# Performance work log

Hardware: AMD Instinct MI355X
Metric: run time of the kernel (lower is better)

Reference implementation:

```python
import jax, jax.numpy as jnp
import numpy as np

# EISANI constants (inference path, dense non-EI weights, static connections)
NUM_BITS = 16        # EISANITABcontinuousVarEncodingNumBits
K_SYN = 32           # numberOfSynapsesPerSegment
SEGMENTS = 2         # numberOfSegmentsPerNeuron
THETA = 8            # segment activation threshold (synapse-count based)
H = 4096             # hiddenLayerSize
F = 128              # numberOfFeatures
C = 10               # numberOfClasses
B = 64               # batch


def _make_weight(key, h, s, p):
    """Dense weight [h, s, p] with exactly K_SYN nonzero +/-1 synapses per segment
    (mirrors _initialise_layer_weights dense non-EI branch)."""
    k1, k2 = jax.random.split(key)
    cols = jax.random.randint(k1, (h, s, K_SYN), 0, p)
    signs = jnp.where(jax.random.bernoulli(k2, 0.5, (h, s, K_SYN)), 1.0, -1.0).astype(jnp.float32)
    hh = jnp.arange(h)[:, None, None]
    ss = jnp.arange(s)[None, :, None]
    return jnp.zeros((h, s, p), jnp.float32).at[hh, ss, cols].set(signs)


def setup_inputs() -> dict:
    key = jax.random.key(0)
    kx, k0, k1, k2, ko = jax.random.split(key, 5)
    x = jax.random.uniform(kx, (B, F), dtype=jnp.float32)
    W0 = _make_weight(k0, H, SEGMENTS, F * NUM_BITS)
    W1 = _make_weight(k1, H, SEGMENTS, H)
    W2 = _make_weight(k2, H, SEGMENTS, H)
    outW = jax.random.normal(ko, (3, H, C), dtype=jnp.float32) * 0.02
    return {"x": x, "W0": W0, "W1": W1, "W2": W2, "outW": outW}


def _encode(x):
    # thermometer (graded) encoding of continuous vars into NUM_BITS binary bits
    thresholds = (jnp.arange(NUM_BITS, dtype=jnp.float32) + 1.0) / (NUM_BITS + 1.0)
    bits = (x[:, :, None] >= thresholds).astype(jnp.float32)  # [B, F, NUM_BITS]
    return bits.reshape(x.shape[0], -1)  # [B, F*NUM_BITS]


def reference(x, W0, W1, W2, outW):
    acts = _encode(x)  # [B, P0]
    layer_acts = []
    for W in (W0, W1, W2):
        # segment membrane sums over binary presynaptic activations
        z = jnp.einsum('bp,hsp->bhs', acts, W)  # [B, H, S]
        # neuron fires if ANY segment reaches threshold
        fired = jnp.any(z >= THETA, axis=-1)
        acts = fired.astype(jnp.float32)  # binary activation [B, H]
        layer_acts.append(acts)
    stacked = jnp.stack(layer_acts)  # [L, B, H]
    out = jnp.einsum('lbh,lhc->bc', stacked, outW)  # class scores [B, C]
    return out
```

## Files before the change

kernel.cpp:

```cpp
#include <hip/hip_runtime.h>
#include <hip/hip_bf16.h>

typedef unsigned long long u64;

#define H_SZ 4096
#define NBITS 16
#define NFEAT 128
#define NCLS 10
#define THETA 8


__global__ void encode_kernel(const float* __restrict__ x, u64* __restrict__ actp0) {
    int idx = blockIdx.x * blockDim.x + threadIdx.x;
    if (idx >= 32 * 64) return;
    int wword = idx >> 6;
    int b = idx & 63;
    int c = wword >> 2, j = wword & 3;
    u64 word = 0;
    for (int i = 0; i < 64; i++) {
        int p = c * 256 + 4 * i + j;
        int f = p >> 4, t = p & 15;
        float thr = (t + 1.0f) / (NBITS + 1.0f);
        if (x[b * NFEAT + f] >= thr) word |= (1ULL << i);
    }
    actp0[wword * 64 + b] = word;
}

template <int NCH, int ROWS>
__global__ __launch_bounds__(256, 4) void layer_kernel(const float* __restrict__ W,
                                                       const u64* __restrict__ actp,
                                                       u64* __restrict__ ballots) {
    constexpr int NW = NCH * 4;
    constexpr int G = 8;
    constexpr int TG = ROWS * NCH / G;
    __shared__ u64 lds[NW * 64];
    int tid = threadIdx.x;
    for (int i = tid; i < NW * 64; i += 256) lds[i] = actp[i];
    __syncthreads();

    int lane = tid & 63;
    int wave = blockIdx.x * 4 + (tid >> 6);
    int wid0 = wave * ROWS;
    const float4* base = (const float4*)(W + (size_t)wid0 * (NCH * 256)) + lane;

    float4 A[G], B[G];
    #pragma unroll
    for (int k = 0; k < G; k++) A[k] = base[k * 64];

    int z = 0;
    #pragma unroll
    for (int g = 0; g < TG; g++) {
        float4* cur = (g & 1) ? B : A;
        float4* nxt = (g & 1) ? A : B;
        if (g + 1 < TG) {
            #pragma unroll
            for (int k = 0; k < G; k++) nxt[k] = base[((g + 1) * G + k) * 64];
        }
        #pragma unroll
        for (int k = 0; k < G; k++) {
            int c = (g * G + k) % NCH;
            float4 v = cur[k];
            u64 p0 = __ballot(v.x > 0.0f);
            u64 n0 = __ballot(v.x < 0.0f);
            u64 p1 = __ballot(v.y > 0.0f);
            u64 n1 = __ballot(v.y < 0.0f);
            u64 p2 = __ballot(v.z > 0.0f);
            u64 n2 = __ballot(v.z < 0.0f);
            u64 p3 = __ballot(v.w > 0.0f);
            u64 n3 = __ballot(v.w < 0.0f);
            u64 a0 = lds[(c * 4 + 0) * 64 + lane];
            u64 a1 = lds[(c * 4 + 1) * 64 + lane];
            u64 a2 = lds[(c * 4 + 2) * 64 + lane];
            u64 a3 = lds[(c * 4 + 3) * 64 + lane];
            z += __builtin_popcountll(a0 & p0) - __builtin_popcountll(a0 & n0)
               + __builtin_popcountll(a1 & p1) - __builtin_popcountll(a1 & n1)
               + __builtin_popcountll(a2 & p2) - __builtin_popcountll(a2 & n2)
               + __builtin_popcountll(a3 & p3) - __builtin_popcountll(a3 & n3);
        }
        if (((g + 1) * G) % NCH == 0) {
            u64 fz = __ballot(z >= THETA);
            int r = ((g + 1) * G) / NCH - 1;
            if (lane == 0) ballots[wid0 + r] = fz;
            z = 0;
        }
    }
}

__global__ void transpose_kernel(const u64* __restrict__ ballots,
                                 u64* __restrict__ f,
                                 u64* __restrict__ actp) {
    __shared__ u64 lds[256];
    int c = blockIdx.x;
    int tid = threadIdx.x;
    int h = c * 256 + tid;
    u64 fh = ballots[2 * h] | ballots[2 * h + 1];
    f[h] = fh;
    lds[tid] = fh;
    __syncthreads();
    int j = tid >> 6, b = tid & 63;
    u64 word = 0;
    #pragma unroll 8
    for (int i = 0; i < 64; i++)
        word |= ((lds[4 * i + j] >> b) & 1ULL) << i;
    actp[(c * 4 + j) * 64 + b] = word;
}

__global__ void output_kernel(const float* __restrict__ outW,
                              const u64* __restrict__ f,
                              float* __restrict__ out) {
    int tid = threadIdx.x;
    int lane = tid & 63;
    int wid = blockIdx.x * 4 + (tid >> 6);
    int l = wid / (NCLS * 64);
    int rem = wid % (NCLS * 64);
    int c = rem / 64;
    int chunk = rem % 64;
    const u64* fl = f + l * H_SZ;
    int h0 = chunk * 64;
    float acc = 0.0f;
    #pragma unroll 8
    for (int h = h0; h < h0 + 64; h++) {
        float wv = outW[((size_t)(l * H_SZ + h)) * NCLS + c];
        u64 ball = fl[h];
        if ((ball >> lane) & 1ULL) acc += wv;
    }
    atomicAdd(&out[lane * NCLS + c], acc);
}

extern "C" void kernel_launch(void* const* d_in, const int* in_sizes, int n_in,
                              void* d_out, int out_size, void* d_ws, size_t ws_size,
                              hipStream_t stream) {
    const float* x    = (const float*)d_in[0];
    const float* W0   = (const float*)d_in[1];
    const float* W1   = (const float*)d_in[2];
    const float* W2   = (const float*)d_in[3];
    const float* outW = (const float*)d_in[4];
    float* out = (float*)d_out;

    char* ws = (char*)d_ws;
    u64* actp0   = (u64*)(ws);
    u64* actp1   = (u64*)(ws + 16384);
    u64* actp2   = (u64*)(ws + 49152);
    u64* ballots = (u64*)(ws + 81920);
    u64* f       = (u64*)(ws + 147456);
    u64* scratch = (u64*)(ws + 245760);

    hipMemsetAsync(d_out, 0, (size_t)out_size * sizeof(float), stream);

    encode_kernel<<<8, 256, 0, stream>>>(x, actp0);

    layer_kernel<8, 2><<<1024, 256, 0, stream>>>(W0, actp0, ballots);
    transpose_kernel<<<16, 256, 0, stream>>>(ballots, f + 0 * H_SZ, actp1);

    layer_kernel<16, 2><<<1024, 256, 0, stream>>>(W1, actp1, ballots);
    transpose_kernel<<<16, 256, 0, stream>>>(ballots, f + 1 * H_SZ, actp2);

    layer_kernel<16, 2><<<1024, 256, 0, stream>>>(W2, actp2, ballots);
    transpose_kernel<<<16, 256, 0, stream>>>(ballots, f + 2 * H_SZ, scratch);

    output_kernel<<<480, 256, 0, stream>>>(outW, f, out);
}
```

Before: 395.6 us.

## Stream all layer weights in one kernel, compress W1/W2 to sign bitmasks

Replaces the three per-layer weight-streaming kernels with one kernel that computes layer 0 and, in the same launch, converts W1 and W2 into packed positive/negative sign bitmasks that do not depend on earlier activations. Layers 1 and 2 then run a small kernel that reads only the compact masks plus activations from LDS. The goal is to read all weight bytes in one fully parallel pass without dependency stalls between layers, so the later layers become cheap. This adds mask writes to workspace at fixed 4MB/16MB offsets and assumes the workspace is large enough.

```diff
diff --git a/kernel.cpp b/kernel.cpp
--- a/kernel.cpp
+++ b/kernel.cpp
@@ -26,63 +26,137 @@
     actp0[wword * 64 + b] = word;
 }
 
-template <int NCH, int ROWS>
-__global__ __launch_bounds__(256, 4) void layer_kernel(const float* __restrict__ W,
-                                                       const u64* __restrict__ actp,
-                                                       u64* __restrict__ ballots) {
-    constexpr int NW = NCH * 4;
+__global__ __launch_bounds__(256, 4) void stream_kernel(const float* __restrict__ W0,
+                                                        const float* __restrict__ W1,
+                                                        const float* __restrict__ W2,
+                                                        const u64* __restrict__ actp0,
+                                                        u64* __restrict__ ballots,
+                                                        u64* __restrict__ mask1,
+                                                        u64* __restrict__ mask2) {
     constexpr int G = 8;
-    constexpr int TG = ROWS * NCH / G;
-    __shared__ u64 lds[NW * 64];
-    int tid = threadIdx.x;
-    for (int i = tid; i < NW * 64; i += 256) lds[i] = actp[i];
+    __shared__ u64 lds[2048];
+    int tid = threadIdx.x;
+    int lane = tid & 63;
+    int warp = tid >> 6;
+    int bid = blockIdx.x;
+
+    if (bid < 512) {
+        for (int i = tid; i < 2048; i += 256) lds[i] = actp0[i];
+        __syncthreads();
+
+        int wave = bid * 4 + warp;
+        int wid0 = wave * 4;
+        const float4* base = (const float4*)(W0 + (size_t)wid0 * 2048) + lane;
+
+        float4 A[G], B[G];
+        #pragma unroll
+        for (int k = 0; k < G; k++) A[k] = base[k * 64];
+
+        #pragma unroll
+        for (int g = 0; g < 4; g++) {
+            float4* cur = (g & 1) ? B : A;
+            float4* nxt = (g & 1) ? A : B;
+            if (g + 1 < 4) {
+                #pragma unroll
+                for (int k = 0; k < G; k++) nxt[k] = base[((g + 1) * G + k) * 64];
+            }
+            int z = 0;
+            #pragma unroll
+            for (int k = 0; k < G; k++) {
+                float4 v = cur[k];
+                u64 p0 = __ballot(v.x > 0.0f);
+                u64 n0 = __ballot(v.x < 0.0f);
+                u64 p1 = __ballot(v.y > 0.0f);
+                u64 n1 = __ballot(v.y < 0.0f);
+                u64 p2 = __ballot(v.z > 0.0f);
+                u64 n2 = __ballot(v.z < 0.0f);
+                u64 p3 = __ballot(v.w > 0.0f);
+                u64 n3 = __ballot(v.w < 0.0f);
+                u64 a0 = lds[(k * 4 + 0) * 64 + lane];
+                u64 a1 = lds[(k * 4 + 1) * 64 + lane];
+                u64 a2 = lds[(k * 4 + 2) * 64 + lane];
+                u64 a3 = lds[(k * 4 + 3) * 64 + lane];
+                z += __builtin_popcountll(a0 & p0) - __builtin_popcountll(a0 & n0)
+                   + __builtin_popcountll(a1 & p1) - __builtin_popcountll(a1 & n1)
+                   + __builtin_popcountll(a2 & p2) - __builtin_popcountll(a2 & n2)
+                   + __builtin_popcountll(a3 & p3) - __builtin_popcountll(a3 & n3);
+            }
+            u64 fz = __ballot(z >= THETA);
+            if (lane == 0) ballots[wid0 + g] = fz;
+        }
+    } else {
+        const float* Wsrc = (bid < 1536) ? W1 : W2;
+        u64* masks = (bid < 1536) ? mask1 : mask2;
+        int wave = ((bid < 1536) ? (bid - 512) : (bid - 1536)) * 4 + warp;
+        size_t c0 = (size_t)wave * 32;
+        const float4* base = (const float4*)Wsrc + c0 * 64 + lane;
+
+        float4 A[G], B[G];
+        #pragma unroll
+        for (int k = 0; k < G; k++) A[k] = base[k * 64];
+
+        #pragma unroll
+        for (int g = 0; g < 4; g++) {
+            float4* cur = (g & 1) ? B : A;
+            float4* nxt = (g & 1) ? A : B;
+            if (g + 1 < 4) {
+                #pragma unroll
+                for (int k = 0; k < G; k++) nxt[k] = base[((g + 1) * G + k) * 64];
+            }
+            #pragma unroll
+            for (int k = 0; k < G; k++) {
+                float4 v = cur[k];
+                u64 m0 = __ballot(v.x > 0.0f);
+                u64 m1 = __ballot(v.x < 0.0f);
+                u64 m2 = __ballot(v.y > 0.0f);
+                u64 m3 = __ballot(v.y < 0.0f);
+                u64 m4 = __ballot(v.z > 0.0f);
+                u64 m5 = __ballot(v.z < 0.0f);
+                u64 m6 = __ballot(v.w > 0.0f);
+                u64 m7 = __ballot(v.w < 0.0f);
+                u64 w = m0;
+                w = (lane == 1) ? m1 : w;
+                w = (lane == 2) ? m2 : w;
+                w = (lane == 3) ? m3 : w;
+                w = (lane == 4) ? m4 : w;
+                w = (lane == 5) ? m5 : w;
+                w = (lane == 6) ? m6 : w;
+                w = (lane == 7) ? m7 : w;
+                if (lane < 8) masks[(c0 + g * G + k) * 8 + lane] = w;
+            }
+        }
+    }
+}
+
+__global__ __launch_bounds__(256) void mask_layer_kernel(const u64* __restrict__ masks,
+                                                         const u64* __restrict__ actp,
+                                                         u64* __restrict__ ballots) {
+    __shared__ u64 am[4096];
+    __shared__ u64 mm[2048];
+    int tid = threadIdx.x;
+    int r0 = blockIdx.x * 16;
+    for (int i = tid; i < 4096; i += 256) am[i] = actp[i];
+    for (int i = tid; i < 2048; i += 256) mm[i] = masks[(size_t)r0 * 128 + i];
     __syncthreads();
 
     int lane = tid & 63;
-    int wave = blockIdx.x * 4 + (tid >> 6);
-    int wid0 = wave * ROWS;
-    const float4* base = (const float4*)(W + (size_t)wid0 * (NCH * 256)) + lane;
-
-    float4 A[G], B[G];
+    int warp = tid >> 6;
     #pragma unroll
-    for (int k = 0; k < G; k++) A[k] = base[k * 64];
-
-    int z = 0;
-    #pragma unroll
-    for (int g = 0; g < TG; g++) {
-        float4* cur = (g & 1) ? B : A;
-        float4* nxt = (g & 1) ? A : B;
-        if (g + 1 < TG) {
+    for (int rr = 0; rr < 4; rr++) {
+        int local = warp * 4 + rr;
+        int z = 0;
+        #pragma unroll
+        for (int c = 0; c < 16; c++) {
             #pragma unroll
-            for (int k = 0; k < G; k++) nxt[k] = base[((g + 1) * G + k) * 64];
+            for (int j = 0; j < 4; j++) {
+                u64 p = mm[local * 128 + c * 8 + j * 2];
+                u64 n = mm[local * 128 + c * 8 + j * 2 + 1];
+                u64 a = am[(c * 4 + j) * 64 + lane];
+                z += __builtin_popcountll(a & p) - __builtin_popcountll(a & n);
+            }
         }
-        #pragma unroll
-        for (int k = 0; k < G; k++) {
-            int c = (g * G + k) % NCH;
-            float4 v = cur[k];
-            u64 p0 = __ballot(v.x > 0.0f);
-            u64 n0 = __ballot(v.x < 0.0f);
-            u64 p1 = __ballot(v.y > 0.0f);
-            u64 n1 = __ballot(v.y < 0.0f);
-            u64 p2 = __ballot(v.z > 0.0f);
-            u64 n2 = __ballot(v.z < 0.0f);
-            u64 p3 = __ballot(v.w > 0.0f);
-            u64 n3 = __ballot(v.w < 0.0f);
-            u64 a0 = lds[(c * 4 + 0) * 64 + lane];
-            u64 a1 = lds[(c * 4 + 1) * 64 + lane];
-            u64 a2 = lds[(c * 4 + 2) * 64 + lane];
-            u64 a3 = lds[(c * 4 + 3) * 64 + lane];
-            z += __builtin_popcountll(a0 & p0) - __builtin_popcountll(a0 & n0)
-               + __builtin_popcountll(a1 & p1) - __builtin_popcountll(a1 & n1)
-               + __builtin_popcountll(a2 & p2) - __builtin_popcountll(a2 & n2)
-               + __builtin_popcountll(a3 & p3) - __builtin_popcountll(a3 & n3);
-        }
-        if (((g + 1) * G) % NCH == 0) {
-            u64 fz = __ballot(z >= THETA);
-            int r = ((g + 1) * G) / NCH - 1;
-            if (lane == 0) ballots[wid0 + r] = fz;
-            z = 0;
-        }
+        u64 fz = __ballot(z >= THETA);
+        if (lane == 0) ballots[r0 + local] = fz;
     }
 }
 
@@ -144,18 +218,21 @@
     u64* ballots = (u64*)(ws + 81920);
     u64* f       = (u64*)(ws + 147456);
     u64* scratch = (u64*)(ws + 245760);
+    u64* mask1   = (u64*)(ws + (4u  << 20));
+    u64* mask2   = (u64*)(ws + (16u << 20));
 
     hipMemsetAsync(d_out, 0, (size_t)out_size * sizeof(float), stream);
 
     encode_kernel<<<8, 256, 0, stream>>>(x, actp0);
 
-    layer_kernel<8, 2><<<1024, 256, 0, stream>>>(W0, actp0, ballots);
+    stream_kernel<<<2560, 256, 0, stream>>>(W0, W1, W2, actp0, ballots, mask1, mask2);
+
     transpose_kernel<<<16, 256, 0, stream>>>(ballots, f + 0 * H_SZ, actp1);
-
-    layer_kernel<16, 2><<<1024, 256, 0, stream>>>(W1, actp1, ballots);
+    mask_layer_kernel<<<512, 256, 0, stream>>>(mask1, actp1, ballots);
+
     transpose_kernel<<<16, 256, 0, stream>>>(ballots, f + 1 * H_SZ, actp2);
-
-    layer_kernel<16, 2><<<1024, 256, 0, stream>>>(W2, actp2, ballots);
+    mask_layer_kernel<<<512, 256, 0, stream>>>(mask2, actp2, ballots);
+
     transpose_kernel<<<16, 256, 0, stream>>>(ballots, f + 2 * H_SZ, scratch);
 
     output_kernel<<<480, 256, 0, stream>>>(outW, f, out);
```

Result: slower. 423.1 us (+6.9%).
